# Kernel tuning notes

Hardware: AMD Instinct MI355X
Metric: run time of the kernel (lower is better)

## Reference

```python
import jax
import jax.numpy as jnp
import numpy as np
from jax import lax

B = 256
H = W = 64
N_ACTIONS = 18
N_EXPERTS = 8
HIDDEN = 1024
LATENT = 256
EXPERT_DIM = 512
TOP_K = 2
CONV_OUT = 64 * H * W  # padding=1, k=3 convs preserve HxW


def setup_inputs() -> dict:
    key = jax.random.key(0)
    ks = jax.random.split(key, 18)

    def rn(k, shape, fan_in):
        # kaiming-ish scale, keeps activations sane
        return jax.random.normal(k, shape, jnp.float32) * np.float32(np.sqrt(2.0 / fan_in))

    return {
        "pixel_obs": jax.random.normal(ks[0], (B, 1, H, W), jnp.float32),
        # conv weights in torch OIHW layout
        "conv1_w": rn(ks[1], (16, 1, 3, 3), 9),
        "conv1_b": jnp.zeros((16,), jnp.float32),
        "conv2_w": rn(ks[2], (32, 16, 3, 3), 16 * 9),
        "conv2_b": jnp.zeros((32,), jnp.float32),
        "conv3_w": rn(ks[3], (64, 32, 3, 3), 32 * 9),
        "conv3_b": jnp.zeros((64,), jnp.float32),
        # linear weights stored [in, out]
        "fc1_w": rn(ks[4], (CONV_OUT, HIDDEN), CONV_OUT),
        "fc1_b": jnp.zeros((HIDDEN,), jnp.float32),
        "fc2_w": rn(ks[5], (HIDDEN, LATENT), HIDDEN),
        "fc2_b": jnp.zeros((LATENT,), jnp.float32),
        "gate_w": rn(ks[6], (LATENT, N_EXPERTS), LATENT),
        "gate_b": jnp.zeros((N_EXPERTS,), jnp.float32),
        # all experts stacked: [E, in, out]
        "exp_w1": rn(ks[7], (N_EXPERTS, LATENT, EXPERT_DIM), LATENT),
        "exp_b1": jnp.zeros((N_EXPERTS, EXPERT_DIM), jnp.float32),
        "exp_w2": rn(ks[8], (N_EXPERTS, EXPERT_DIM, N_ACTIONS), EXPERT_DIM),
        "exp_b2": jnp.zeros((N_EXPERTS, N_ACTIONS), jnp.float32),
    }


def _conv(x, w, b):
    y = lax.conv_general_dilated(
        x, w, window_strides=(1, 1), padding="SAME",
        dimension_numbers=("NCHW", "OIHW", "NCHW"))
    return jax.nn.relu(y + b[None, :, None, None])


def reference(pixel_obs, conv1_w, conv1_b, conv2_w, conv2_b, conv3_w, conv3_b,
              fc1_w, fc1_b, fc2_w, fc2_b, gate_w, gate_b,
              exp_w1, exp_b1, exp_w2, exp_b2):
    h = _conv(pixel_obs, conv1_w, conv1_b)
    h = _conv(h, conv2_w, conv2_b)
    h = _conv(h, conv3_w, conv3_b)          # [B, 64, H, W]
    flat = h.reshape(h.shape[0], -1)         # NCHW flatten matches torch .view
    s = jax.nn.relu(flat @ fc1_w + fc1_b)
    s = jax.nn.relu(s @ fc2_w + fc2_b)       # shared features [B, LATENT]

    gate_probs = jax.nn.softmax(s @ gate_w + gate_b, axis=1)  # [B, E]
    top_v, top_i = lax.top_k(gate_probs, TOP_K)               # [B, K]
    top_v = top_v / jnp.sum(top_v, axis=1, keepdims=True)

    # dense per-expert compute, as in the original (all experts on all tokens)
    eh = jax.nn.relu(jnp.einsum("bl,elh->beh", s, exp_w1) + exp_b1[None])
    eo = jnp.einsum("beh,eha->bea", eh, exp_w2) + exp_b2[None]  # [B, E, A]

    # fused gather + weighted combine (replaces the python double loop)
    sel = jnp.take_along_axis(eo, top_i[:, :, None], axis=1)    # [B, K, A]
    action_logits = jnp.sum(top_v[:, :, None] * sel, axis=1)    # [B, A]
    return action_logits, gate_probs
```

## Files before the change

### kernel.cpp

```cpp
#include <hip/hip_runtime.h>

typedef _Float16 f16x8 __attribute__((ext_vector_type(8)));
typedef _Float16 f16x4 __attribute__((ext_vector_type(4)));
typedef float f32x4 __attribute__((ext_vector_type(4)));

__global__ void prepack_w(const float* __restrict__ w, _Float16* __restrict__ ph,
                          _Float16* __restrict__ pl, int COUT, int CIN, int KPAD)
{
  const int idx = blockIdx.x * 256 + threadIdx.x;
  const int KTOT = 3 * KPAD;
  if (idx >= COUT * KTOT) return;
  const int oc = idx / KTOT;
  const int rem = idx - oc * KTOT;
  const int y = rem / KPAD;
  const int kk = rem - y * KPAD;
  float v = 0.f;
  if (kk < 3 * CIN) {
    const int tx = kk / CIN;
    const int ic = kk - tx * CIN;
    v = w[((size_t)oc * CIN + ic) * 9 + y * 3 + tx];
  }
  const _Float16 h = (_Float16)v;
  ph[idx] = h;
  pl[idx] = (_Float16)((v - (float)h) * 2048.0f);
}

__global__ __launch_bounds__(256)
void conv1_k(const float* __restrict__ obs, const float* __restrict__ w,
             const float* __restrict__ bias, _Float16* __restrict__ outh,
             _Float16* __restrict__ outl)
{
  const int rg = blockIdx.x;
  const int b = blockIdx.y;
  const int tid = threadIdx.x;
  const int lr = tid >> 6;
  const int col = tid & 63;
  __shared__ float xs[6][66];
  __shared__ float wb[9][16];
  for (int idx = tid; idx < 6 * 66; idx += 256) {
    const int r = idx / 66, c = idx - (idx / 66) * 66;
    const int gr = rg * 4 - 1 + r, gc = c - 1;
    xs[r][c] = (gr >= 0 && gr < 64 && gc >= 0 && gc < 64)
                   ? obs[(size_t)b * 4096 + gr * 64 + gc] : 0.f;
  }
  if (tid < 144) wb[tid / 16][tid & 15] = w[(tid & 15) * 9 + tid / 16];
  __syncthreads();
  float acc[16];
#pragma unroll
  for (int o = 0; o < 16; ++o) acc[o] = bias[o];
#pragma unroll
  for (int ty = 0; ty < 3; ++ty)
#pragma unroll
    for (int tx = 0; tx < 3; ++tx) {
      const float x = xs[lr + ty][col + tx];
#pragma unroll
      for (int o = 0; o < 16; ++o) acc[o] = fmaf(x, wb[ty * 3 + tx][o], acc[o]);
    }
  const size_t base = ((size_t)(b * 64 + rg * 4 + lr) * 64 + col) * 16;
#pragma unroll
  for (int o = 0; o < 16; ++o) {
    const float v = fmaxf(acc[o], 0.f);
    const _Float16 h = (_Float16)v;
    outh[base + o] = h;
    outl[base + o] = (_Float16)((v - (float)h) * 2048.0f);
  }
}

template<int CIN, int COUT, bool NCHW_OUT>
__global__ __launch_bounds__(256)
void conv_mfma(const _Float16* __restrict__ inh, const _Float16* __restrict__ inl,
               const _Float16* __restrict__ wph, const _Float16* __restrict__ wpl,
               const float* __restrict__ bias,
               _Float16* __restrict__ outh, _Float16* __restrict__ outl)
{
  constexpr int KFX = (3 * CIN + 31) / 32;
  constexpr int KPAD = KFX * 32;
  constexpr int KTOT = 3 * KPAD;
  constexpr int CP = CIN + 8;
  constexpr int NF = COUT / 32;
  constexpr int STO = NCHW_OUT ? COUT : 1;
  constexpr int STP = NCHW_OUT ? 136 : 8;
  const int rp = blockIdx.x;
  const int b  = blockIdx.y;
  const int r0 = rp * 2;
  const int tid = threadIdx.x;
  const int lane = tid & 63;
  const int wid = tid >> 6;
  const int wm = wid >> 1;
  const int wn = wid & 1;

  __shared__ _Float16 xh[4][68][CP];
  __shared__ _Float16 xl[4][68][CP];
  __shared__ _Float16 st_h[STO][STP];
  __shared__ _Float16 st_l[STO][STP];

  constexpr int CH = CIN / 8;
  for (int idx = tid; idx < 4 * 68 * CH; idx += 256) {
    const int r = idx / (68 * CH);
    const int rem = idx - r * 68 * CH;
    const int hc = rem / CH;
    const int ch = rem - hc * CH;
    const int gr = r0 - 1 + r;
    const int gc = hc - 1;
    uint4 vh = {0, 0, 0, 0}, vl = {0, 0, 0, 0};
    if (gr >= 0 && gr < 64 && gc >= 0 && gc < 64) {
      const size_t base = ((size_t)(b * 64 + gr) * 64 + gc) * CIN + ch * 8;
      vh = *(const uint4*)(inh + base);
      vl = *(const uint4*)(inl + base);
    }
    *(uint4*)&xh[r][hc][ch * 8] = vh;
    *(uint4*)&xl[r][hc][ch * 8] = vl;
  }
  __syncthreads();

  f32x4 accm[4][NF];
  f32x4 accc[4][NF];
#pragma unroll
  for (int mf = 0; mf < 4; ++mf)
#pragma unroll
    for (int nf = 0; nf < NF; ++nf) { accm[mf][nf] = {}; accc[mf][nf] = {}; }

  const int lm = lane & 15;
  const int ch8 = (lane >> 4) * 8;

#pragma unroll
  for (int kf = 0; kf < 3 * KFX; ++kf) {
    const int y = kf / KFX;
    const int fx = kf - y * KFX;
    const int kk = fx * 32 + ch8;
    f16x8 bh[NF], bl[NF];
#pragma unroll
    for (int nf = 0; nf < NF; ++nf) {
      const int oc = wn * (16 * NF) + nf * 16 + lm;
      bh[nf] = *(const f16x8*)(wph + (size_t)oc * KTOT + kf * 32 + ch8);
      bl[nf] = *(const f16x8*)(wpl + (size_t)oc * KTOT + kf * 32 + ch8);
    }
#pragma unroll
    for (int mf = 0; mf < 4; ++mf) {
      const int col = mf * 16 + lm;
      const f16x8 ah = *(const f16x8*)&xh[wm + y][col + kk / CIN][kk % CIN];
      const f16x8 al = *(const f16x8*)&xl[wm + y][col + kk / CIN][kk % CIN];
#pragma unroll
      for (int nf = 0; nf < NF; ++nf) {
        accm[mf][nf] = __builtin_amdgcn_mfma_f32_16x16x32_f16(ah, bh[nf], accm[mf][nf], 0, 0, 0);
        accc[mf][nf] = __builtin_amdgcn_mfma_f32_16x16x32_f16(ah, bl[nf], accc[mf][nf], 0, 0, 0);
        accc[mf][nf] = __builtin_amdgcn_mfma_f32_16x16x32_f16(al, bh[nf], accc[mf][nf], 0, 0, 0);
      }
    }
  }

  if constexpr (NCHW_OUT) {
#pragma unroll
    for (int nf = 0; nf < NF; ++nf) {
      const int oc = wn * (16 * NF) + nf * 16 + lm;
      const float bv = bias[oc];
#pragma unroll
      for (int mf = 0; mf < 4; ++mf) {
        f16x4 hv, lv;
#pragma unroll
        for (int r = 0; r < 4; ++r) {
          const float v = fmaxf(accm[mf][nf][r] + accc[mf][nf][r] * (1.0f / 2048.0f) + bv, 0.f);
          const _Float16 h = (_Float16)v;
          hv[r] = h;
          lv[r] = (_Float16)((v - (float)h) * 2048.0f);
        }
        const int px = wm * 64 + mf * 16 + (lane >> 4) * 4;
        *(f16x4*)&st_h[oc][px] = hv;
        *(f16x4*)&st_l[oc][px] = lv;
      }
    }
    __syncthreads();
    const int oc2 = tid >> 2;
    const int seg = tid & 3;
    const size_t gb = ((size_t)b * COUT + oc2) * 4096 + r0 * 64 + seg * 32;
#pragma unroll
    for (int j2 = 0; j2 < 4; ++j2) {
      *(uint4*)(outh + gb + j2 * 8) = *(const uint4*)&st_h[oc2][seg * 32 + j2 * 8];
      *(uint4*)(outl + gb + j2 * 8) = *(const uint4*)&st_l[oc2][seg * 32 + j2 * 8];
    }
  } else {
    const int orow = r0 + wm;
#pragma unroll
    for (int nf = 0; nf < NF; ++nf) {
      const int oc = wn * (16 * NF) + nf * 16 + lm;
      const float bv = bias[oc];
#pragma unroll
      for (int mf = 0; mf < 4; ++mf) {
#pragma unroll
        for (int r = 0; r < 4; ++r) {
          const int x = mf * 16 + (lane >> 4) * 4 + r;
          const float v = fmaxf(accm[mf][nf][r] + accc[mf][nf][r] * (1.0f / 2048.0f) + bv, 0.f);
          const _Float16 h = (_Float16)v;
          const size_t oi = ((size_t)(b * 64 + orow) * 64 + x) * COUT + oc;
          outh[oi] = h;
          outl[oi] = (_Float16)((v - (float)h) * 2048.0f);
        }
      }
    }
  }
}

__global__ __launch_bounds__(512, 2)
void fc1_gemm_v4(const _Float16* __restrict__ Ahi, const _Float16* __restrict__ Alo,
                 const float* __restrict__ W, float* __restrict__ P)
{
  const int sk = blockIdx.x;
  const int nt = blockIdx.y;
  const int nc0 = nt * 128;
  const int tid = threadIdx.x;
  const int lane = tid & 63;
  const int wid = tid >> 6;
  const int wm = wid >> 1;
  const int wn = wid & 1;

  __shared__ _Float16 Ah[2][256][32];
  __shared__ _Float16 Al[2][256][32];
  __shared__ _Float16 Bh[2][128][32];
  __shared__ _Float16 Bl[2][128][32];

  f32x4 accm[4][4] = {};
  f32x4 accc[4][4] = {};

  const int nl = tid & 127;
  const int kq = tid >> 7;
  const int bslot = kq ^ ((nl >> 1) & 3);

  const size_t kbase = (size_t)sk * 8192;
  constexpr int NIT = 256;

  const int Rbase = wid * 32;
  const int lrow0 = Rbase + (lane >> 2);
  const int lrow1 = Rbase + 16 + (lane >> 2);
  const int sd = lane & 3;
  const int ssrc0 = sd ^ ((lrow0 >> 1) & 3);
  const int ssrc1 = sd ^ ((lrow1 >> 1) & 3);
  const size_t goff0 = (size_t)lrow0 * 262144 + ssrc0 * 8;
  const size_t goff1 = (size_t)lrow1 * 262144 + ssrc1 * 8;

#define ISSUE_A(p, k0)                                                                     \
  {                                                                                        \
    __builtin_amdgcn_global_load_lds(                                                      \
        (const __attribute__((address_space(1))) unsigned int*)(Ahi + goff0 + (k0)),       \
        (__attribute__((address_space(3))) unsigned int*)&Ah[p][Rbase][0], 16, 0, 0);      \
    __builtin_amdgcn_global_load_lds(                                                      \
        (const __attribute__((address_space(1))) unsigned int*)(Ahi + goff1 + (k0)),       \
        (__attribute__((address_space(3))) unsigned int*)&Ah[p][Rbase + 16][0], 16, 0, 0); \
    __builtin_amdgcn_global_load_lds(                                                      \
        (const __attribute__((address_space(1))) unsigned int*)(Alo + goff0 + (k0)),       \
        (__attribute__((address_space(3))) unsigned int*)&Al[p][Rbase][0], 16, 0, 0);      \
    __builtin_amdgcn_global_load_lds(                                                      \
        (const __attribute__((address_space(1))) unsigned int*)(Alo + goff1 + (k0)),       \
        (__attribute__((address_space(3))) unsigned int*)&Al[p][Rbase + 16][0], 16, 0, 0); \
  }

#define LOAD_W(k0, wr)                                                     \
  {                                                                        \
    const size_t jb = (k0) + kq * 8;                                       \
    _Pragma("unroll") for (int i = 0; i < 8; ++i) {                        \
      wr[i] = W[(jb + i) * 1024 + nc0 + nl];                               \
    }                                                                      \
  }

#define WRITE_B(p, wr)                                                     \
  {                                                                        \
    f16x8 hv, lv;                                                          \
    _Pragma("unroll") for (int i = 0; i < 8; ++i) {                        \
      const _Float16 h = (_Float16)wr[i];                                  \
      hv[i] = h;                                                           \
      lv[i] = (_Float16)((wr[i] - (float)h) * 2048.0f);                    \
    }                                                                      \
    *(f16x8*)&Bh[p][nl][bslot * 8] = hv;                                   \
    *(f16x8*)&Bl[p][nl][bslot * 8] = lv;                                   \
  }

#define COMPUTE(p)                                                                          \
  {                                                                                         \
    const int q = lane >> 4;                                                                \
    f16x8 ah[4], al[4], bh[4], bl[4];                                                       \
    _Pragma("unroll") for (int mf = 0; mf < 4; ++mf) {                                      \
      const int r = wm * 64 + mf * 16 + (lane & 15);                                        \
      const int s = (q ^ ((r >> 1) & 3)) * 8;                                               \
      ah[mf] = *(const f16x8*)&Ah[p][r][s];                                                 \
      al[mf] = *(const f16x8*)&Al[p][r][s];                                                 \
    }                                                                                       \
    _Pragma("unroll") for (int nf = 0; nf < 4; ++nf) {                                      \
      const int n = wn * 64 + nf * 16 + (lane & 15);                                        \
      const int s = (q ^ ((n >> 1) & 3)) * 8;                                               \
      bh[nf] = *(const f16x8*)&Bh[p][n][s];                                                 \
      bl[nf] = *(const f16x8*)&Bl[p][n][s];                                                 \
    }                                                                                       \
    _Pragma("unroll") for (int mf = 0; mf < 4; ++mf)                                        \
      _Pragma("unroll") for (int nf = 0; nf < 4; ++nf) {                                    \
        accm[mf][nf] = __builtin_amdgcn_mfma_f32_16x16x32_f16(ah[mf], bh[nf], accm[mf][nf], 0, 0, 0); \
        accc[mf][nf] = __builtin_amdgcn_mfma_f32_16x16x32_f16(ah[mf], bl[nf], accc[mf][nf], 0, 0, 0); \
        accc[mf][nf] = __builtin_amdgcn_mfma_f32_16x16x32_f16(al[mf], bh[nf], accc[mf][nf], 0, 0, 0); \
      }                                                                                     \
  }

  {
    float wr[8];
    LOAD_W(kbase, wr);
    ISSUE_A(0, kbase);
    WRITE_B(0, wr);
    LOAD_W(kbase + 32, wr);
    ISSUE_A(1, kbase + 32);
    asm volatile("s_waitcnt vmcnt(12)\n\ts_waitcnt lgkmcnt(0)\n\ts_barrier" ::: "memory");
  }

  {
    float wr[8];
    LOAD_W(kbase + 32, wr);
    for (int it = 0; it < NIT - 1; ++it) {
      const int cur = it & 1;
      COMPUTE(cur);
      WRITE_B(cur ^ 1, wr);
      asm volatile("s_waitcnt vmcnt(0)\n\ts_waitcnt lgkmcnt(0)\n\ts_barrier" ::: "memory");
      if (it + 2 < NIT) {
        const size_t k2 = kbase + (size_t)(it + 2) * 32;
        LOAD_W(k2, wr);
        ISSUE_A(cur, k2);
      }
    }
    COMPUTE((NIT - 1) & 1);
  }
#undef ISSUE_A
#undef LOAD_W
#undef WRITE_B
#undef COMPUTE

#pragma unroll
  for (int mf = 0; mf < 4; ++mf) {
    const int rbase = wm * 64 + mf * 16 + ((lane >> 4) << 2);
#pragma unroll
    for (int nf = 0; nf < 4; ++nf) {
      const int c = nc0 + wn * 64 + nf * 16 + (lane & 15);
#pragma unroll
      for (int r = 0; r < 4; ++r)
        P[((size_t)sk * 256 + rbase + r) * 1024 + c] =
            accm[mf][nf][r] + accc[mf][nf][r] * (1.0f / 2048.0f);
    }
  }
}

__global__ __launch_bounds__(256)
void fc1_reduce(const float* __restrict__ P, const float* __restrict__ bias,
                float* __restrict__ s1)
{
  const int idx = blockIdx.x * 256 + threadIdx.x;
  const int n = idx & 1023;
  float a = bias[n];
#pragma unroll 8
  for (int sk = 0; sk < 32; ++sk) a += P[(size_t)sk * 262144 + idx];
  s1[idx] = fmaxf(a, 0.f);
}

__global__ __launch_bounds__(256)
void fc2_k(const float* __restrict__ s1, const float* __restrict__ w,
           const float* __restrict__ b, float* __restrict__ s2)
{
  const int bb = blockIdx.x;
  const int t = threadIdx.x;
  __shared__ float xr[1024];
  for (int i = t; i < 1024; i += 256) xr[i] = s1[bb * 1024 + i];
  __syncthreads();
  float a0 = b[t], a1 = 0.f, a2 = 0.f, a3 = 0.f;
#pragma unroll 4
  for (int k = 0; k < 1024; k += 4) {
    a0 += xr[k + 0] * w[(k + 0) * 256 + t];
    a1 += xr[k + 1] * w[(k + 1) * 256 + t];
    a2 += xr[k + 2] * w[(k + 2) * 256 + t];
    a3 += xr[k + 3] * w[(k + 3) * 256 + t];
  }
  s2[bb * 256 + t] = fmaxf(a0 + a1 + a2 + a3, 0.f);
}

__global__ __launch_bounds__(64)
void gate_k(const float* __restrict__ s2, const float* __restrict__ gw,
            const float* __restrict__ gb, float* __restrict__ gate_out,
            int* __restrict__ topi, float* __restrict__ topv)
{
  const int bb = blockIdx.x;
  const int l = threadIdx.x;
  float part[8] = {};
  for (int k = l; k < 256; k += 64) {
    const float x = s2[bb * 256 + k];
#pragma unroll
    for (int e = 0; e < 8; ++e) part[e] += x * gw[k * 8 + e];
  }
#pragma unroll
  for (int off = 32; off > 0; off >>= 1)
#pragma unroll
    for (int e = 0; e < 8; ++e) part[e] += __shfl_down(part[e], off);

  if (l == 0) {
    float lg[8];
    float m = -1e30f;
#pragma unroll
    for (int e = 0; e < 8; ++e) { lg[e] = part[e] + gb[e]; m = fmaxf(m, lg[e]); }
    float s = 0.f;
    float p[8];
#pragma unroll
    for (int e = 0; e < 8; ++e) { p[e] = expf(lg[e] - m); s += p[e]; }
#pragma unroll
    for (int e = 0; e < 8; ++e) { p[e] = p[e] / s; gate_out[bb * 8 + e] = p[e]; }
    int i0 = 0;
#pragma unroll
    for (int e = 1; e < 8; ++e) if (p[e] > p[i0]) i0 = e;
    int i1 = (i0 == 0) ? 1 : 0;
#pragma unroll
    for (int e = 0; e < 8; ++e) if (e != i0 && p[e] > p[i1]) i1 = e;
    const float v0 = p[i0], v1 = p[i1];
    topi[bb * 2 + 0] = i0; topi[bb * 2 + 1] = i1;
    topv[bb * 2 + 0] = v0 / (v0 + v1); topv[bb * 2 + 1] = v1 / (v0 + v1);
  }
}

__global__ __launch_bounds__(256)
void expert_k(const float* __restrict__ s2, const float* __restrict__ w1,
              const float* __restrict__ b1, const float* __restrict__ w2,
              const float* __restrict__ b2, const int* __restrict__ topi,
              const float* __restrict__ topv, float* __restrict__ out)
{
  const int bb = blockIdx.x;
  const int t = threadIdx.x;
  __shared__ float xr[256];
  __shared__ float eh[512];
  __shared__ float partial[18][8];
  xr[t] = s2[bb * 256 + t];
  float logit = 0.f;
  for (int kk = 0; kk < 2; ++kk) {
    __syncthreads();
    const int e = topi[bb * 2 + kk];
    const float tv = topv[bb * 2 + kk];
    const float* W1 = w1 + (size_t)e * 256 * 512;
    float a0 = b1[e * 512 + t], a1 = b1[e * 512 + 256 + t];
#pragma unroll 4
    for (int k = 0; k < 256; ++k) {
      const float x = xr[k];
      a0 = fmaf(x, W1[k * 512 + t], a0);
      a1 = fmaf(x, W1[k * 512 + 256 + t], a1);
    }
    eh[t] = fmaxf(a0, 0.f);
    eh[256 + t] = fmaxf(a1, 0.f);
    __syncthreads();
    if (t < 144) {
      const int a = t >> 3, q2 = t & 7;
      const float* W2 = w2 + (size_t)e * 512 * 18;
      float pp = 0.f;
      for (int h = q2 * 64; h < q2 * 64 + 64; ++h) pp = fmaf(eh[h], W2[h * 18 + a], pp);
      partial[a][q2] = pp;
    }
    __syncthreads();
    if (t < 18) {
      float s = b2[e * 18 + t];
#pragma unroll
      for (int q2 = 0; q2 < 8; ++q2) s += partial[t][q2];
      logit = fmaf(tv, s, logit);
    }
  }
  if (t < 18) out[bb * 18 + t] = logit;
}

extern "C" void kernel_launch(void* const* d_in, const int* in_sizes, int n_in,
                              void* d_out, int out_size, void* d_ws, size_t ws_size,
                              hipStream_t stream) {
  const float* obs     = (const float*)d_in[0];
  const float* conv1_w = (const float*)d_in[1];
  const float* conv1_b = (const float*)d_in[2];
  const float* conv2_w = (const float*)d_in[3];
  const float* conv2_b = (const float*)d_in[4];
  const float* conv3_w = (const float*)d_in[5];
  const float* conv3_b = (const float*)d_in[6];
  const float* fc1_w   = (const float*)d_in[7];
  const float* fc1_b   = (const float*)d_in[8];
  const float* fc2_w   = (const float*)d_in[9];
  const float* fc2_b   = (const float*)d_in[10];
  const float* gate_w  = (const float*)d_in[11];
  const float* gate_b  = (const float*)d_in[12];
  const float* exp_w1  = (const float*)d_in[13];
  const float* exp_b1  = (const float*)d_in[14];
  const float* exp_w2  = (const float*)d_in[15];
  const float* exp_b2  = (const float*)d_in[16];

  char* ws = (char*)d_ws;
  const size_t MB = 1ull << 20;
  const size_t KB = 1ull << 10;
  _Float16* act1h = (_Float16*)(ws);
  _Float16* act1l = (_Float16*)(ws + 32 * MB);
  _Float16* act2h = (_Float16*)(ws + 64 * MB);
  _Float16* act2l = (_Float16*)(ws + 128 * MB);
  _Float16* act3h = (_Float16*)(ws + 192 * MB);
  _Float16* act3l = (_Float16*)(ws + 320 * MB);
  float*    P     = (float*)(ws);
  _Float16* wp2h  = (_Float16*)(ws + 448 * MB);
  _Float16* wp2l  = (_Float16*)(ws + 448 * MB + 64 * KB);
  _Float16* wp3h  = (_Float16*)(ws + 448 * MB + 128 * KB);
  _Float16* wp3l  = (_Float16*)(ws + 448 * MB + 192 * KB);
  float*    s2    = (float*)(ws + 448 * MB + 256 * KB);
  int*      topi  = (int*)(ws + 448 * MB + 512 * KB);
  float*    topv  = (float*)(ws + 448 * MB + 516 * KB);
  float*    s1    = (float*)(ws + 449 * MB);
  float*    out   = (float*)d_out;

  prepack_w<<<(32 * 192 + 255) / 256, 256, 0, stream>>>(conv2_w, wp2h, wp2l, 32, 16, 64);
  prepack_w<<<(64 * 288 + 255) / 256, 256, 0, stream>>>(conv3_w, wp3h, wp3l, 64, 32, 96);

  conv1_k<<<dim3(16, 256), 256, 0, stream>>>(obs, conv1_w, conv1_b, act1h, act1l);
  conv_mfma<16, 32, false><<<dim3(32, 256), 256, 0, stream>>>(act1h, act1l, wp2h, wp2l, conv2_b, act2h, act2l);
  conv_mfma<32, 64, true ><<<dim3(32, 256), 256, 0, stream>>>(act2h, act2l, wp3h, wp3l, conv3_b, act3h, act3l);

  fc1_gemm_v4<<<dim3(32, 8), 512, 0, stream>>>(act3h, act3l, fc1_w, P);
  fc1_reduce<<<1024, 256, 0, stream>>>(P, fc1_b, s1);
  fc2_k<<<256, 256, 0, stream>>>(s1, fc2_w, fc2_b, s2);
  gate_k<<<256, 64, 0, stream>>>(s2, gate_w, gate_b, out + 256 * 18, topi, topv);
  expert_k<<<256, 256, 0, stream>>>(s2, exp_w1, exp_b1, exp_w2, exp_b2, topi, topv, out);
}
```

Measured before the change: 981.2 us.

## Split fc1 GEMM over M into two 128-row tiles for more blocks

```diff
diff --git a/kernel.cpp b/kernel.cpp
--- a/kernel.cpp
+++ b/kernel.cpp
@@ -200,26 +200,27 @@
   }
 }
 
-__global__ __launch_bounds__(512, 2)
-void fc1_gemm_v4(const _Float16* __restrict__ Ahi, const _Float16* __restrict__ Alo,
+__global__ __launch_bounds__(512, 4)
+void fc1_gemm_v5(const _Float16* __restrict__ Ahi, const _Float16* __restrict__ Alo,
                  const float* __restrict__ W, float* __restrict__ P)
 {
   const int sk = blockIdx.x;
   const int nt = blockIdx.y;
+  const int mt = blockIdx.z;
   const int nc0 = nt * 128;
   const int tid = threadIdx.x;
   const int lane = tid & 63;
   const int wid = tid >> 6;
-  const int wm = wid >> 1;
-  const int wn = wid & 1;
-
-  __shared__ _Float16 Ah[2][256][32];
-  __shared__ _Float16 Al[2][256][32];
+  const int wm = wid >> 2;
+  const int wn = wid & 3;
+
+  __shared__ _Float16 Ah[2][128][32];
+  __shared__ _Float16 Al[2][128][32];
   __shared__ _Float16 Bh[2][128][32];
   __shared__ _Float16 Bl[2][128][32];
 
-  f32x4 accm[4][4] = {};
-  f32x4 accc[4][4] = {};
+  f32x4 accm[4][2] = {};
+  f32x4 accc[4][2] = {};
 
   const int nl = tid & 127;
   const int kq = tid >> 7;
@@ -228,29 +229,19 @@
   const size_t kbase = (size_t)sk * 8192;
   constexpr int NIT = 256;
 
-  const int Rbase = wid * 32;
-  const int lrow0 = Rbase + (lane >> 2);
-  const int lrow1 = Rbase + 16 + (lane >> 2);
+  const int lrow = wid * 16 + (lane >> 2);
   const int sd = lane & 3;
-  const int ssrc0 = sd ^ ((lrow0 >> 1) & 3);
-  const int ssrc1 = sd ^ ((lrow1 >> 1) & 3);
-  const size_t goff0 = (size_t)lrow0 * 262144 + ssrc0 * 8;
-  const size_t goff1 = (size_t)lrow1 * 262144 + ssrc1 * 8;
+  const int ssrc = sd ^ ((lrow >> 1) & 3);
+  const size_t goff = ((size_t)(mt * 128 + lrow)) * 262144 + ssrc * 8;
 
 #define ISSUE_A(p, k0)                                                                     \
   {                                                                                        \
     __builtin_amdgcn_global_load_lds(                                                      \
-        (const __attribute__((address_space(1))) unsigned int*)(Ahi + goff0 + (k0)),       \
-        (__attribute__((address_space(3))) unsigned int*)&Ah[p][Rbase][0], 16, 0, 0);      \
+        (const __attribute__((address_space(1))) unsigned int*)(Ahi + goff + (k0)),        \
+        (__attribute__((address_space(3))) unsigned int*)&Ah[p][wid * 16][0], 16, 0, 0);   \
     __builtin_amdgcn_global_load_lds(                                                      \
-        (const __attribute__((address_space(1))) unsigned int*)(Ahi + goff1 + (k0)),       \
-        (__attribute__((address_space(3))) unsigned int*)&Ah[p][Rbase + 16][0], 16, 0, 0); \
-    __builtin_amdgcn_global_load_lds(                                                      \
-        (const __attribute__((address_space(1))) unsigned int*)(Alo + goff0 + (k0)),       \
-        (__attribute__((address_space(3))) unsigned int*)&Al[p][Rbase][0], 16, 0, 0);      \
-    __builtin_amdgcn_global_load_lds(                                                      \
-        (const __attribute__((address_space(1))) unsigned int*)(Alo + goff1 + (k0)),       \
-        (__attribute__((address_space(3))) unsigned int*)&Al[p][Rbase + 16][0], 16, 0, 0); \
+        (const __attribute__((address_space(1))) unsigned int*)(Alo + goff + (k0)),        \
+        (__attribute__((address_space(3))) unsigned int*)&Al[p][wid * 16][0], 16, 0, 0);   \
   }
 
 #define LOAD_W(k0, wr)                                                     \
@@ -276,25 +267,27 @@
 #define COMPUTE(p)                                                                          \
   {                                                                                         \
     const int q = lane >> 4;                                                                \
-    f16x8 ah[4], al[4], bh[4], bl[4];                                                       \
+    f16x8 ah[4], al[4], bh[2], bl[2];                                                       \
     _Pragma("unroll") for (int mf = 0; mf < 4; ++mf) {                                      \
       const int r = wm * 64 + mf * 16 + (lane & 15);                                        \
       const int s = (q ^ ((r >> 1) & 3)) * 8;                                               \
       ah[mf] = *(const f16x8*)&Ah[p][r][s];                                                 \
       al[mf] = *(const f16x8*)&Al[p][r][s];                                                 \
     }                                                                                       \
-    _Pragma("unroll") for (int nf = 0; nf < 4; ++nf) {                                      \
-      const int n = wn * 64 + nf * 16 + (lane & 15);                                        \
+    _Pragma("unroll") for (int nf = 0; nf < 2; ++nf) {                                      \
+      const int n = wn * 32 + nf * 16 + (lane & 15);                                        \
       const int s = (q ^ ((n >> 1) & 3)) * 8;                                               \
       bh[nf] = *(const f16x8*)&Bh[p][n][s];                                                 \
       bl[nf] = *(const f16x8*)&Bl[p][n][s];                                                 \
     }                                                                                       \
+    __builtin_amdgcn_s_setprio(1);                                                          \
     _Pragma("unroll") for (int mf = 0; mf < 4; ++mf)                                        \
-      _Pragma("unroll") for (int nf = 0; nf < 4; ++nf) {                                    \
+      _Pragma("unroll") for (int nf = 0; nf < 2; ++nf) {                                    \
         accm[mf][nf] = __builtin_amdgcn_mfma_f32_16x16x32_f16(ah[mf], bh[nf], accm[mf][nf], 0, 0, 0); \
         accc[mf][nf] = __builtin_amdgcn_mfma_f32_16x16x32_f16(ah[mf], bl[nf], accc[mf][nf], 0, 0, 0); \
         accc[mf][nf] = __builtin_amdgcn_mfma_f32_16x16x32_f16(al[mf], bh[nf], accc[mf][nf], 0, 0, 0); \
       }                                                                                     \
+    __builtin_amdgcn_s_setprio(0);                                                          \
   }
 
   {
@@ -304,7 +297,7 @@
     WRITE_B(0, wr);
     LOAD_W(kbase + 32, wr);
     ISSUE_A(1, kbase + 32);
-    asm volatile("s_waitcnt vmcnt(12)\n\ts_waitcnt lgkmcnt(0)\n\ts_barrier" ::: "memory");
+    asm volatile("s_waitcnt vmcnt(10)\n\ts_waitcnt lgkmcnt(0)\n\ts_barrier" ::: "memory");
   }
 
   {
@@ -330,10 +323,10 @@
 
 #pragma unroll
   for (int mf = 0; mf < 4; ++mf) {
-    const int rbase = wm * 64 + mf * 16 + ((lane >> 4) << 2);
-#pragma unroll
-    for (int nf = 0; nf < 4; ++nf) {
-      const int c = nc0 + wn * 64 + nf * 16 + (lane & 15);
+    const int rbase = mt * 128 + wm * 64 + mf * 16 + ((lane >> 4) << 2);
+#pragma unroll
+    for (int nf = 0; nf < 2; ++nf) {
+      const int c = nc0 + wn * 32 + nf * 16 + (lane & 15);
 #pragma unroll
       for (int r = 0; r < 4; ++r)
         P[((size_t)sk * 256 + rbase + r) * 1024 + c] =
@@ -509,7 +502,7 @@
   conv_mfma<16, 32, false><<<dim3(32, 256), 256, 0, stream>>>(act1h, act1l, wp2h, wp2l, conv2_b, act2h, act2l);
   conv_mfma<32, 64, true ><<<dim3(32, 256), 256, 0, stream>>>(act2h, act2l, wp3h, wp3l, conv3_b, act3h, act3l);
 
-  fc1_gemm_v4<<<dim3(32, 8), 512, 0, stream>>>(act3h, act3l, fc1_w, P);
+  fc1_gemm_v5<<<dim3(32, 8, 2), 512, 0, stream>>>(act3h, act3l, fc1_w, P);
   fc1_reduce<<<1024, 256, 0, stream>>>(P, fc1_b, s1);
   fc2_k<<<256, 256, 0, stream>>>(s1, fc2_w, fc2_b, s2);
   gate_k<<<256, 64, 0, stream>>>(s2, gate_w, gate_b, out + 256 * 18, topi, topv);
```

Measured after the change: 1.289 ms. +31.4%, slower.

## Load fc1 A fragments directly from global into registers, dropping LDS staging

Applied to the files above, without the earlier changes.

```diff
diff --git a/kernel.cpp b/kernel.cpp
--- a/kernel.cpp
+++ b/kernel.cpp
@@ -201,7 +201,7 @@
 }
 
 __global__ __launch_bounds__(512, 2)
-void fc1_gemm_v4(const _Float16* __restrict__ Ahi, const _Float16* __restrict__ Alo,
+void fc1_gemm_v6(const _Float16* __restrict__ Ahi, const _Float16* __restrict__ Alo,
                  const float* __restrict__ W, float* __restrict__ P)
 {
   const int sk = blockIdx.x;
@@ -213,8 +213,6 @@
   const int wm = wid >> 1;
   const int wn = wid & 1;
 
-  __shared__ _Float16 Ah[2][256][32];
-  __shared__ _Float16 Al[2][256][32];
   __shared__ _Float16 Bh[2][128][32];
   __shared__ _Float16 Bl[2][128][32];
 
@@ -224,65 +222,49 @@
   const int nl = tid & 127;
   const int kq = tid >> 7;
   const int bslot = kq ^ ((nl >> 1) & 3);
+  const int q = lane >> 4;
 
   const size_t kbase = (size_t)sk * 8192;
   constexpr int NIT = 256;
 
-  const int Rbase = wid * 32;
-  const int lrow0 = Rbase + (lane >> 2);
-  const int lrow1 = Rbase + 16 + (lane >> 2);
-  const int sd = lane & 3;
-  const int ssrc0 = sd ^ ((lrow0 >> 1) & 3);
-  const int ssrc1 = sd ^ ((lrow1 >> 1) & 3);
-  const size_t goff0 = (size_t)lrow0 * 262144 + ssrc0 * 8;
-  const size_t goff1 = (size_t)lrow1 * 262144 + ssrc1 * 8;
-
-#define ISSUE_A(p, k0)                                                                     \
-  {                                                                                        \
-    __builtin_amdgcn_global_load_lds(                                                      \
-        (const __attribute__((address_space(1))) unsigned int*)(Ahi + goff0 + (k0)),       \
-        (__attribute__((address_space(3))) unsigned int*)&Ah[p][Rbase][0], 16, 0, 0);      \
-    __builtin_amdgcn_global_load_lds(                                                      \
-        (const __attribute__((address_space(1))) unsigned int*)(Ahi + goff1 + (k0)),       \
-        (__attribute__((address_space(3))) unsigned int*)&Ah[p][Rbase + 16][0], 16, 0, 0); \
-    __builtin_amdgcn_global_load_lds(                                                      \
-        (const __attribute__((address_space(1))) unsigned int*)(Alo + goff0 + (k0)),       \
-        (__attribute__((address_space(3))) unsigned int*)&Al[p][Rbase][0], 16, 0, 0);      \
-    __builtin_amdgcn_global_load_lds(                                                      \
-        (const __attribute__((address_space(1))) unsigned int*)(Alo + goff1 + (k0)),       \
-        (__attribute__((address_space(3))) unsigned int*)&Al[p][Rbase + 16][0], 16, 0, 0); \
-  }
-
-#define LOAD_W(k0, wr)                                                     \
-  {                                                                        \
-    const size_t jb = (k0) + kq * 8;                                       \
-    _Pragma("unroll") for (int i = 0; i < 8; ++i) {                        \
-      wr[i] = W[(jb + i) * 1024 + nc0 + nl];                               \
-    }                                                                      \
-  }
-
-#define WRITE_B(p, wr)                                                     \
-  {                                                                        \
-    f16x8 hv, lv;                                                          \
-    _Pragma("unroll") for (int i = 0; i < 8; ++i) {                        \
-      const _Float16 h = (_Float16)wr[i];                                  \
-      hv[i] = h;                                                           \
-      lv[i] = (_Float16)((wr[i] - (float)h) * 2048.0f);                    \
-    }                                                                      \
-    *(f16x8*)&Bh[p][nl][bslot * 8] = hv;                                   \
-    *(f16x8*)&Bl[p][nl][bslot * 8] = lv;                                   \
-  }
-
-#define COMPUTE(p)                                                                          \
+  unsigned aoff[4];
+#pragma unroll
+  for (int mf = 0; mf < 4; ++mf) {
+    const int row = wm * 64 + mf * 16 + (lane & 15);
+    aoff[mf] = (unsigned)row * 262144u + (unsigned)q * 8u;
+  }
+
+#define LOAD_A(dh, dl, k0)                                                  \
+  {                                                                         \
+    _Pragma("unroll") for (int mf = 0; mf < 4; ++mf) {                      \
+      dh[mf] = *(const f16x8*)(Ahi + (size_t)aoff[mf] + (k0));              \
+      dl[mf] = *(const f16x8*)(Alo + (size_t)aoff[mf] + (k0));              \
+    }                                                                       \
+  }
+
+#define LOAD_W(k0, wr)                                                      \
+  {                                                                         \
+    const size_t jb = (k0) + kq * 8;                                        \
+    _Pragma("unroll") for (int i = 0; i < 8; ++i) {                         \
+      wr[i] = W[(jb + i) * 1024 + nc0 + nl];                                \
+    }                                                                       \
+  }
+
+#define WRITE_B(p, wr)                                                      \
+  {                                                                         \
+    f16x8 hv, lv;                                                           \
+    _Pragma("unroll") for (int i = 0; i < 8; ++i) {                         \
+      const _Float16 h = (_Float16)wr[i];                                   \
+      hv[i] = h;                                                            \
+      lv[i] = (_Float16)((wr[i] - (float)h) * 2048.0f);                     \
+    }                                                                       \
+    *(f16x8*)&Bh[p][nl][bslot * 8] = hv;                                    \
+    *(f16x8*)&Bl[p][nl][bslot * 8] = lv;                                    \
+  }
+
+#define COMPUTE(p, ah, al)                                                                  \
   {                                                                                         \
-    const int q = lane >> 4;                                                                \
-    f16x8 ah[4], al[4], bh[4], bl[4];                                                       \
-    _Pragma("unroll") for (int mf = 0; mf < 4; ++mf) {                                      \
-      const int r = wm * 64 + mf * 16 + (lane & 15);                                        \
-      const int s = (q ^ ((r >> 1) & 3)) * 8;                                               \
-      ah[mf] = *(const f16x8*)&Ah[p][r][s];                                                 \
-      al[mf] = *(const f16x8*)&Al[p][r][s];                                                 \
-    }                                                                                       \
+    f16x8 bh[4], bl[4];                                                                     \
     _Pragma("unroll") for (int nf = 0; nf < 4; ++nf) {                                      \
       const int n = wn * 64 + nf * 16 + (lane & 15);                                        \
       const int s = (q ^ ((n >> 1) & 3)) * 8;                                               \
@@ -297,33 +279,30 @@
       }                                                                                     \
   }
 
-  {
-    float wr[8];
-    LOAD_W(kbase, wr);
-    ISSUE_A(0, kbase);
-    WRITE_B(0, wr);
-    LOAD_W(kbase + 32, wr);
-    ISSUE_A(1, kbase + 32);
-    asm volatile("s_waitcnt vmcnt(12)\n\ts_waitcnt lgkmcnt(0)\n\ts_barrier" ::: "memory");
-  }
-
-  {
-    float wr[8];
-    LOAD_W(kbase + 32, wr);
-    for (int it = 0; it < NIT - 1; ++it) {
-      const int cur = it & 1;
-      COMPUTE(cur);
-      WRITE_B(cur ^ 1, wr);
-      asm volatile("s_waitcnt vmcnt(0)\n\ts_waitcnt lgkmcnt(0)\n\ts_barrier" ::: "memory");
-      if (it + 2 < NIT) {
-        const size_t k2 = kbase + (size_t)(it + 2) * 32;
-        LOAD_W(k2, wr);
-        ISSUE_A(cur, k2);
-      }
-    }
-    COMPUTE((NIT - 1) & 1);
-  }
-#undef ISSUE_A
+  f16x8 fAh[4], fAl[4];
+  f16x8 fBh[4], fBl[4];
+  float wr[8];
+
+  LOAD_A(fAh, fAl, kbase);
+  LOAD_W(kbase, wr);
+  WRITE_B(0, wr);
+  LOAD_A(fBh, fBl, kbase + 32);
+  LOAD_W(kbase + 32, wr);
+  asm volatile("s_waitcnt lgkmcnt(0)\n\ts_barrier" ::: "memory");
+
+  for (int it = 0; it < NIT; it += 2) {
+    COMPUTE(0, fAh, fAl);
+    if (it + 2 < NIT) LOAD_A(fAh, fAl, kbase + (size_t)(it + 2) * 32);
+    WRITE_B(1, wr);
+    asm volatile("s_waitcnt lgkmcnt(0)\n\ts_barrier" ::: "memory");
+    if (it + 2 < NIT) LOAD_W(kbase + (size_t)(it + 2) * 32, wr);
+    COMPUTE(1, fBh, fBl);
+    if (it + 3 < NIT) LOAD_A(fBh, fBl, kbase + (size_t)(it + 3) * 32);
+    if (it + 2 < NIT) WRITE_B(0, wr);
+    asm volatile("s_waitcnt lgkmcnt(0)\n\ts_barrier" ::: "memory");
+    if (it + 3 < NIT) LOAD_W(kbase + (size_t)(it + 3) * 32, wr);
+  }
+#undef LOAD_A
 #undef LOAD_W
 #undef WRITE_B
 #undef COMPUTE
@@ -509,7 +488,7 @@
   conv_mfma<16, 32, false><<<dim3(32, 256), 256, 0, stream>>>(act1h, act1l, wp2h, wp2l, conv2_b, act2h, act2l);
   conv_mfma<32, 64, true ><<<dim3(32, 256), 256, 0, stream>>>(act2h, act2l, wp3h, wp3l, conv3_b, act3h, act3l);
 
-  fc1_gemm_v4<<<dim3(32, 8), 512, 0, stream>>>(act3h, act3l, fc1_w, P);
+  fc1_gemm_v6<<<dim3(32, 8), 512, 0, stream>>>(act3h, act3l, fc1_w, P);
   fc1_reduce<<<1024, 256, 0, stream>>>(P, fc1_b, s1);
   fc2_k<<<256, 256, 0, stream>>>(s1, fc2_w, fc2_b, s2);
   gate_k<<<256, 64, 0, stream>>>(s2, gate_w, gate_b, out + 256 * 18, topi, topv);
```

Result: slower. 1.417 ms (+44.4%).
